# Kernel optimization log

Measured on AMD Instinct MI355X. Metric: run time of the kernel, lower is better.

Reference implementation:

```python
import jax, jax.numpy as jnp
import numpy as np

B, T, D, H = 4, 2048, 1024, 16
DH = D // H


def setup_inputs() -> dict:
    key = jax.random.key(0)
    ks = jax.random.split(key, 5)
    x = jax.random.normal(ks[0], (B, T, D), dtype=jnp.float32)
    W_qkv = jax.random.normal(ks[1], (D, 3 * D), dtype=jnp.float32) * 0.02
    b_qkv = jax.random.normal(ks[2], (3 * D,), dtype=jnp.float32) * 0.02
    W_o = jax.random.normal(ks[3], (D, D), dtype=jnp.float32) * 0.02
    b_o = jax.random.normal(ks[4], (D,), dtype=jnp.float32) * 0.02
    return {"x": x, "W_qkv": W_qkv, "b_qkv": b_qkv, "W_o": W_o, "b_o": b_o}


def reference(x, W_qkv, b_qkv, W_o, b_o):
    b, t, d = x.shape
    qkv = x @ W_qkv + b_qkv                      # [b, t, 3*d]
    # 'b t (k h dh) -> k b h t dh'
    qkv = qkv.reshape(b, t, 3, H, DH).transpose(2, 0, 3, 1, 4)
    q, k, v = qkv[0], qkv[1], qkv[2]             # each [b, h, t, dh]
    scores = jnp.einsum('bhqd,bhkd->bhqk', q, k) / jnp.sqrt(jnp.float32(DH))
    causal_mask = jnp.triu(jnp.ones((t, t), dtype=bool), k=1)  # True above diag
    scores = jnp.where(causal_mask, -jnp.inf, scores)
    attn = jax.nn.softmax(scores, axis=-1)       # [b, h, t, t]
    o = jnp.einsum('bhqk,bhkd->bqhd', attn, v).reshape(b, t, d)
    return o @ W_o + b_o
```

## Files before the change

kernel.cpp:

```cpp
#include <hip/hip_runtime.h>
#include <hip/hip_bf16.h>

typedef __attribute__((ext_vector_type(8))) short bh8;
typedef __attribute__((ext_vector_type(4))) float f32x4;

#define GBL(p) (const __attribute__((address_space(1))) void*)(p)
#define LDSP(p) (__attribute__((address_space(3))) void*)(p)

__device__ __forceinline__ ushort f2bf(float f){
  union { float f; unsigned u; } v; v.f = f;
  unsigned u = v.u;
  return (ushort)((u + 0x7fffu + ((u >> 16) & 1u)) >> 16);
}

__global__ __launch_bounds__(256) void cast_x_kernel(const float4* __restrict__ in,
                                                     ushort* __restrict__ out){
  int i = blockIdx.x * 256 + threadIdx.x;
  float4 v = in[i];
  ushort4 o;
  o.x = f2bf(v.x); o.y = f2bf(v.y); o.z = f2bf(v.z); o.w = f2bf(v.w);
  *(ushort4*)&out[(size_t)i * 4] = o;
}

__global__ __launch_bounds__(256) void transpose_cast_kernel(const float* __restrict__ in,
                                                             ushort* __restrict__ out,
                                                             int R, int C){
  __shared__ float tile[32][33];
  int bx = blockIdx.x * 32;
  int by = blockIdx.y * 32;
  int tx = threadIdx.x, ty = threadIdx.y;
  #pragma unroll
  for (int i = 0; i < 32; i += 8)
    tile[ty + i][tx] = in[(size_t)(by + ty + i) * C + bx + tx];
  __syncthreads();
  #pragma unroll
  for (int i = 0; i < 32; i += 8)
    out[(size_t)(bx + ty + i) * R + by + tx] = f2bf(tile[tx][ty + i]);
}

__global__ __launch_bounds__(256) void gemm_qkv_kernel(
    const ushort* __restrict__ A,
    const ushort* __restrict__ Bt,
    const float* __restrict__ bias,
    ushort* __restrict__ Qd, ushort* __restrict__ Kd, ushort* __restrict__ Vt)
{
  constexpr int K = 1024;
  __shared__ ushort sA[8192];
  __shared__ ushort sB[8192];
  const int tid = threadIdx.x;
  const int lane = tid & 63, wave = tid >> 6;
  const int quad = lane >> 4, l16 = lane & 15;
  const int rx7 = l16 & 7;
  const int wm = (wave >> 1) * 64, wn = (wave & 1) * 64;
  const size_t aBase = (size_t)blockIdx.x * 128 * K;
  const size_t bBase = (size_t)blockIdx.y * 128 * K;
  f32x4 acc[4][4] = {};
  for (int k0 = 0; k0 < K; k0 += 64){
    #pragma unroll
    for (int c = 0; c < 4; c++){
      int u = c * 256 + tid;
      int row = u >> 3, cu = (u & 7) ^ (row & 7);
      __builtin_amdgcn_global_load_lds(GBL(A + aBase + (size_t)row * K + k0 + cu * 8),
                                       LDSP(&sA[u * 8]), 16, 0, 0);
      __builtin_amdgcn_global_load_lds(GBL(Bt + bBase + (size_t)row * K + k0 + cu * 8),
                                       LDSP(&sB[u * 8]), 16, 0, 0);
    }
    __syncthreads();
    #pragma unroll
    for (int ks = 0; ks < 2; ks++){
      bh8 af[4], bf[4];
      #pragma unroll
      for (int i = 0; i < 4; i++){
        int row = wm + i * 16 + l16;
        af[i] = *(const bh8*)&sA[row * 64 + (((ks * 4 + quad) ^ rx7) << 3)];
      }
      #pragma unroll
      for (int j = 0; j < 4; j++){
        int row = wn + j * 16 + l16;
        bf[j] = *(const bh8*)&sB[row * 64 + (((ks * 4 + quad) ^ rx7) << 3)];
      }
      #pragma unroll
      for (int i = 0; i < 4; i++)
        #pragma unroll
        for (int j = 0; j < 4; j++)
          acc[i][j] = __builtin_amdgcn_mfma_f32_16x16x32_bf16(af[i], bf[j], acc[i][j], 0, 0, 0);
    }
    __syncthreads();
  }
  const int whichBlk = (blockIdx.y * 128) >> 10;
  #pragma unroll
  for (int i = 0; i < 4; i++){
    int mg = blockIdx.x * 128 + wm + i * 16 + quad * 4;
    int bb = mg >> 11, t0 = mg & 2047;
    #pragma unroll
    for (int j = 0; j < 4; j++){
      int ng = blockIdx.y * 128 + wn + j * 16 + l16;
      float bv = bias[ng];
      int h = (ng >> 6) & 15;
      int dh = ng & 63;
      if (whichBlk == 2){
        ushort4 o;
        o.x = f2bf(acc[i][j][0] + bv);
        o.y = f2bf(acc[i][j][1] + bv);
        o.z = f2bf(acc[i][j][2] + bv);
        o.w = f2bf(acc[i][j][3] + bv);
        *(ushort4*)&Vt[((size_t)((bb * 16 + h) * 64 + dh)) * 2048 + t0] = o;
      } else {
        ushort* dst = (whichBlk == 0) ? Qd : Kd;
        float sc = (whichBlk == 0) ? 0.18033688f : 1.0f;
        #pragma unroll
        for (int r = 0; r < 4; r++)
          dst[((size_t)((bb * 16 + h) * 2048 + t0 + r) << 6) + dh] = f2bf((acc[i][j][r] + bv) * sc);
      }
    }
  }
}

__global__ __launch_bounds__(256, 4) void flash_attn_kernel(
    const ushort* __restrict__ Qd, const ushort* __restrict__ Kd,
    const ushort* __restrict__ Vt, ushort* __restrict__ Od)
{
  __shared__ ushort sK[2][4096];
  __shared__ ushort sV[2][4096];
  __shared__ ushort sP[4][1024];
  const int tid = threadIdx.x;
  const int lane = tid & 63, wave = tid >> 6;
  const int quad = lane >> 4, l16 = lane & 15;
  const int bh = blockIdx.x, pairI = blockIdx.y;
  const size_t base = (size_t)bh * (2048 * 64);
  const float SINIT = -7.2134752f;

  const int p0 = tid, p1 = 256 + tid;
  const int r0 = p0 >> 3, c0 = (p0 & 7) ^ (r0 & 7);
  const int r1 = p1 >> 3, c1 = (p1 & 7) ^ (r1 & 7);
  const ushort* kp0 = Kd + base + r0 * 64 + c0 * 8;
  const ushort* kp1 = Kd + base + r1 * 64 + c1 * 8;
  const ushort* vp0 = Vt + base + (size_t)r0 * 2048 + c0 * 8;
  const ushort* vp1 = Vt + base + (size_t)r1 * 2048 + c1 * 8;

  const int b = bh >> 4, h = bh & 15;

  #pragma unroll 1
  for (int phase = 0; phase < 2; phase++){
    const int qt = phase ? pairI : (31 - pairI);
    const ushort* qrow = Qd + base + (size_t)(qt * 64 + wave * 16 + l16) * 64 + quad * 8;
    bh8 qf0 = *(const bh8*)qrow;
    bh8 qf1 = *(const bh8*)(qrow + 32);

    f32x4 Oacc[4] = {};
    float lpart[4] = {0.f, 0.f, 0.f, 0.f};

    __syncthreads();
    __builtin_amdgcn_global_load_lds(GBL(kp0), LDSP(&sK[0][p0 * 8]), 16, 0, 0);
    __builtin_amdgcn_global_load_lds(GBL(kp1), LDSP(&sK[0][p1 * 8]), 16, 0, 0);
    __builtin_amdgcn_global_load_lds(GBL(vp0), LDSP(&sV[0][p0 * 8]), 16, 0, 0);
    __builtin_amdgcn_global_load_lds(GBL(vp1), LDSP(&sV[0][p1 * 8]), 16, 0, 0);

    #pragma unroll 1
    for (int kt = 0; kt <= qt; kt++){
      const int buf = kt & 1;
      __syncthreads();
      if (kt < qt){
        const int nb = buf ^ 1;
        __builtin_amdgcn_global_load_lds(GBL(kp0 + (kt + 1) * 4096), LDSP(&sK[nb][p0 * 8]), 16, 0, 0);
        __builtin_amdgcn_global_load_lds(GBL(kp1 + (kt + 1) * 4096), LDSP(&sK[nb][p1 * 8]), 16, 0, 0);
        __builtin_amdgcn_global_load_lds(GBL(vp0 + (kt + 1) * 64),   LDSP(&sV[nb][p0 * 8]), 16, 0, 0);
        __builtin_amdgcn_global_load_lds(GBL(vp1 + (kt + 1) * 64),   LDSP(&sV[nb][p1 * 8]), 16, 0, 0);
      }
      f32x4 S[4];
      #pragma unroll
      for (int j = 0; j < 4; j++) S[j] = (f32x4){SINIT, SINIT, SINIT, SINIT};
      #pragma unroll
      for (int ks = 0; ks < 2; ks++){
        bh8 aq = ks ? qf1 : qf0;
        #pragma unroll
        for (int j = 0; j < 4; j++){
          int row = j * 16 + l16;
          int u = row * 8 + ((ks * 4 + quad) ^ (row & 7));
          bh8 bk = *(const bh8*)&sK[buf][u * 8];
          S[j] = __builtin_amdgcn_mfma_f32_16x16x32_bf16(aq, bk, S[j], 0, 0, 0);
        }
      }
      if (kt == qt){
        #pragma unroll
        for (int j = 0; j < 4; j++)
          #pragma unroll
          for (int r = 0; r < 4; r++){
            int relq = wave * 16 + quad * 4 + r;
            int relt = j * 16 + l16;
            if (relt > relq) S[j][r] = -1e30f;
          }
      }
      #pragma unroll
      for (int j = 0; j < 4; j++){
        float pv[4];
        #pragma unroll
        for (int r = 0; r < 4; r++){
          pv[r] = exp2f(S[j][r]);
          lpart[r] += pv[r];
        }
        __hip_bfloat162 pk0 = __float22bfloat162_rn({pv[0], pv[1]});
        __hip_bfloat162 pk1 = __float22bfloat162_rn({pv[2], pv[3]});
        ushort2 w0 = *(ushort2*)&pk0, w1 = *(ushort2*)&pk1;
        ushort w[4] = {w0.x, w0.y, w1.x, w1.y};
        #pragma unroll
        for (int r = 0; r < 4; r++){
          int row = quad * 4 + r;
          int cu = 2 * j + (l16 >> 3);
          int phys = row * 8 + (cu ^ (row & 7));
          sP[wave][phys * 8 + (l16 & 7)] = w[r];
        }
      }
      #pragma unroll
      for (int ks = 0; ks < 2; ks++){
        int up = l16 * 8 + ((ks * 4 + quad) ^ (l16 & 7));
        bh8 ap = *(const bh8*)&sP[wave][up * 8];
        #pragma unroll
        for (int j = 0; j < 4; j++){
          int row = j * 16 + l16;
          int u = row * 8 + ((ks * 4 + quad) ^ (row & 7));
          bh8 bv = *(const bh8*)&sV[buf][u * 8];
          Oacc[j] = __builtin_amdgcn_mfma_f32_16x16x32_bf16(ap, bv, Oacc[j], 0, 0, 0);
        }
      }
    }
    float lr[4];
    #pragma unroll
    for (int r = 0; r < 4; r++){
      float s = lpart[r];
      s += __shfl_xor(s, 1, 64);
      s += __shfl_xor(s, 2, 64);
      s += __shfl_xor(s, 4, 64);
      s += __shfl_xor(s, 8, 64);
      lr[r] = 1.0f / s;
    }
    #pragma unroll
    for (int j = 0; j < 4; j++)
      #pragma unroll
      for (int r = 0; r < 4; r++){
        int qg = qt * 64 + wave * 16 + quad * 4 + r;
        int dh = j * 16 + l16;
        Od[(size_t)(b * 2048 + qg) * 1024 + h * 64 + dh] = f2bf(Oacc[j][r] * lr[r]);
      }
  }
}

__global__ __launch_bounds__(256) void gemm_out_kernel(
    const ushort* __restrict__ A,
    const ushort* __restrict__ Bt,
    const float* __restrict__ bias,
    float* __restrict__ out)
{
  constexpr int K = 1024;
  __shared__ ushort sA[8192];
  __shared__ ushort sB[4096];
  const int tid = threadIdx.x;
  const int lane = tid & 63, wave = tid >> 6;
  const int quad = lane >> 4, l16 = lane & 15;
  const int rx7 = l16 & 7;
  const int wm = (wave >> 1) * 64, wn = (wave & 1) * 32;
  const size_t aBase = (size_t)blockIdx.x * 128 * K;
  const size_t bBase = (size_t)blockIdx.y * 64 * K;
  f32x4 acc[4][2] = {};
  for (int k0 = 0; k0 < K; k0 += 64){
    #pragma unroll
    for (int c = 0; c < 4; c++){
      int u = c * 256 + tid;
      int row = u >> 3, cu = (u & 7) ^ (row & 7);
      __builtin_amdgcn_global_load_lds(GBL(A + aBase + (size_t)row * K + k0 + cu * 8),
                                       LDSP(&sA[u * 8]), 16, 0, 0);
    }
    #pragma unroll
    for (int c = 0; c < 2; c++){
      int u = c * 256 + tid;
      int row = u >> 3, cu = (u & 7) ^ (row & 7);
      __builtin_amdgcn_global_load_lds(GBL(Bt + bBase + (size_t)row * K + k0 + cu * 8),
                                       LDSP(&sB[u * 8]), 16, 0, 0);
    }
    __syncthreads();
    #pragma unroll
    for (int ks = 0; ks < 2; ks++){
      bh8 af[4], bf[2];
      #pragma unroll
      for (int i = 0; i < 4; i++){
        int row = wm + i * 16 + l16;
        af[i] = *(const bh8*)&sA[row * 64 + (((ks * 4 + quad) ^ rx7) << 3)];
      }
      #pragma unroll
      for (int j = 0; j < 2; j++){
        int row = wn + j * 16 + l16;
        bf[j] = *(const bh8*)&sB[row * 64 + (((ks * 4 + quad) ^ rx7) << 3)];
      }
      #pragma unroll
      for (int i = 0; i < 4; i++)
        #pragma unroll
        for (int j = 0; j < 2; j++)
          acc[i][j] = __builtin_amdgcn_mfma_f32_16x16x32_bf16(af[i], bf[j], acc[i][j], 0, 0, 0);
    }
    __syncthreads();
  }
  #pragma unroll
  for (int i = 0; i < 4; i++){
    int gm = blockIdx.x * 128 + wm + i * 16 + quad * 4;
    #pragma unroll
    for (int j = 0; j < 2; j++){
      int ng = blockIdx.y * 64 + wn + j * 16 + l16;
      float bv = bias[ng];
      #pragma unroll
      for (int r = 0; r < 4; r++)
        out[(size_t)(gm + r) * 1024 + ng] = acc[i][j][r] + bv;
    }
  }
}

extern "C" void kernel_launch(void* const* d_in, const int* in_sizes, int n_in,
                              void* d_out, int out_size, void* d_ws, size_t ws_size,
                              hipStream_t stream) {
  const float* x    = (const float*)d_in[0];
  const float* Wqkv = (const float*)d_in[1];
  const float* bqkv = (const float*)d_in[2];
  const float* Wo   = (const float*)d_in[3];
  const float* bo   = (const float*)d_in[4];
  float* out = (float*)d_out;

  char* p = (char*)d_ws;
  ushort* xb  = (ushort*)p;
  ushort* WqT = (ushort*)(p + 16777216);
  ushort* WoT = (ushort*)(p + 16777216 + 6291456);
  ushort* Qd  = (ushort*)(p + 25165824);
  ushort* Kd  = (ushort*)(p + 25165824 + 16777216);
  ushort* Vt  = (ushort*)(p + 25165824 + 33554432);
  ushort* Od  = xb;

  cast_x_kernel<<<8192, 256, 0, stream>>>((const float4*)x, xb);
  transpose_cast_kernel<<<dim3(96, 32), dim3(32, 8), 0, stream>>>(Wqkv, WqT, 1024, 3072);
  transpose_cast_kernel<<<dim3(32, 32), dim3(32, 8), 0, stream>>>(Wo, WoT, 1024, 1024);
  gemm_qkv_kernel<<<dim3(64, 24), 256, 0, stream>>>(xb, WqT, bqkv, Qd, Kd, Vt);
  flash_attn_kernel<<<dim3(64, 16), 256, 0, stream>>>(Qd, Kd, Vt, Od);
  gemm_out_kernel<<<dim3(64, 16), 256, 0, stream>>>(Od, WoT, bo, out);
}
```

Before: 261.1 us.

## Compute transposed scores to keep P in registers, dropping LDS round-trip

The QK^T MFMA now swaps its operands so each lane holds scores for one query row across key positions. The bf16 probabilities can then feed a 16x16x16 MFMA directly as the B operand against V, with no write to and read back from the per-wave sP LDS buffer. The row-sum reduction shrinks to two cross-quad shuffles, and the output is written as packed 4-element stores. The trade is twice as many smaller MFMA instructions for the PV product and narrower 8-byte LDS reads of V, in exchange for less LDS traffic, less LDS footprint and no intra-wave LDS dependency.

New measurement: 288.1 us. 1.1x slower.

```diff
diff --git a/kernel.cpp b/kernel.cpp
--- a/kernel.cpp
+++ b/kernel.cpp
@@ -2,10 +2,17 @@
 #include <hip/hip_bf16.h>
 
 typedef __attribute__((ext_vector_type(8))) short bh8;
+typedef __attribute__((ext_vector_type(4))) short bh4;
 typedef __attribute__((ext_vector_type(4))) float f32x4;
 
 #define GBL(p) (const __attribute__((address_space(1))) void*)(p)
 #define LDSP(p) (__attribute__((address_space(3))) void*)(p)
+
+#if __has_builtin(__builtin_amdgcn_mfma_f32_16x16x16_bf16)
+#define MFMA16(a, b, c) __builtin_amdgcn_mfma_f32_16x16x16_bf16(a, b, c, 0, 0, 0)
+#else
+#define MFMA16(a, b, c) __builtin_amdgcn_mfma_f32_16x16x16bf16_1k(a, b, c, 0, 0, 0)
+#endif
 
 __device__ __forceinline__ ushort f2bf(float f){
   union { float f; unsigned u; } v; v.f = f;
@@ -122,7 +129,6 @@
 {
   __shared__ ushort sK[2][4096];
   __shared__ ushort sV[2][4096];
-  __shared__ ushort sP[4][1024];
   const int tid = threadIdx.x;
   const int lane = tid & 63, wave = tid >> 6;
   const int quad = lane >> 4, l16 = lane & 15;
@@ -148,7 +154,7 @@
     bh8 qf1 = *(const bh8*)(qrow + 32);
 
     f32x4 Oacc[4] = {};
-    float lpart[4] = {0.f, 0.f, 0.f, 0.f};
+    float lsum = 0.f;
 
     __syncthreads();
     __builtin_amdgcn_global_load_lds(GBL(kp0), LDSP(&sK[0][p0 * 8]), 16, 0, 0);
@@ -172,76 +178,61 @@
       for (int j = 0; j < 4; j++) S[j] = (f32x4){SINIT, SINIT, SINIT, SINIT};
       #pragma unroll
       for (int ks = 0; ks < 2; ks++){
-        bh8 aq = ks ? qf1 : qf0;
+        bh8 qk = ks ? qf1 : qf0;
         #pragma unroll
         for (int j = 0; j < 4; j++){
           int row = j * 16 + l16;
           int u = row * 8 + ((ks * 4 + quad) ^ (row & 7));
           bh8 bk = *(const bh8*)&sK[buf][u * 8];
-          S[j] = __builtin_amdgcn_mfma_f32_16x16x32_bf16(aq, bk, S[j], 0, 0, 0);
+          S[j] = __builtin_amdgcn_mfma_f32_16x16x32_bf16(bk, qk, S[j], 0, 0, 0);
         }
       }
       if (kt == qt){
+        const int relq = wave * 16 + l16;
         #pragma unroll
         for (int j = 0; j < 4; j++)
           #pragma unroll
           for (int r = 0; r < 4; r++){
-            int relq = wave * 16 + quad * 4 + r;
-            int relt = j * 16 + l16;
+            int relt = j * 16 + quad * 4 + r;
             if (relt > relq) S[j][r] = -1e30f;
           }
       }
+      bh4 pf[4];
       #pragma unroll
       for (int j = 0; j < 4; j++){
-        float pv[4];
-        #pragma unroll
-        for (int r = 0; r < 4; r++){
-          pv[r] = exp2f(S[j][r]);
-          lpart[r] += pv[r];
+        float pv0 = exp2f(S[j][0]), pv1 = exp2f(S[j][1]);
+        float pv2 = exp2f(S[j][2]), pv3 = exp2f(S[j][3]);
+        lsum += (pv0 + pv1) + (pv2 + pv3);
+        __hip_bfloat162 k0 = __float22bfloat162_rn({pv0, pv1});
+        __hip_bfloat162 k1 = __float22bfloat162_rn({pv2, pv3});
+        ushort2 w0 = *(ushort2*)&k0, w1 = *(ushort2*)&k1;
+        pf[j] = (bh4){(short)w0.x, (short)w0.y, (short)w1.x, (short)w1.y};
+      }
+      #pragma unroll
+      for (int mt = 0; mt < 4; mt++){
+        int row = mt * 16 + l16;
+        #pragma unroll
+        for (int j = 0; j < 4; j++){
+          int cu = j * 2 + (quad >> 1);
+          int idx = (row * 8 + (cu ^ (row & 7))) * 8 + (quad & 1) * 4;
+          bh4 vf = *(const bh4*)&sV[buf][idx];
+          Oacc[mt] = MFMA16(vf, pf[j], Oacc[mt]);
         }
-        __hip_bfloat162 pk0 = __float22bfloat162_rn({pv[0], pv[1]});
-        __hip_bfloat162 pk1 = __float22bfloat162_rn({pv[2], pv[3]});
-        ushort2 w0 = *(ushort2*)&pk0, w1 = *(ushort2*)&pk1;
-        ushort w[4] = {w0.x, w0.y, w1.x, w1.y};
-        #pragma unroll
-        for (int r = 0; r < 4; r++){
-          int row = quad * 4 + r;
-          int cu = 2 * j + (l16 >> 3);
-          int phys = row * 8 + (cu ^ (row & 7));
-          sP[wave][phys * 8 + (l16 & 7)] = w[r];
-        }
-      }
-      #pragma unroll
-      for (int ks = 0; ks < 2; ks++){
-        int up = l16 * 8 + ((ks * 4 + quad) ^ (l16 & 7));
-        bh8 ap = *(const bh8*)&sP[wave][up * 8];
-        #pragma unroll
-        for (int j = 0; j < 4; j++){
-          int row = j * 16 + l16;
-          int u = row * 8 + ((ks * 4 + quad) ^ (row & 7));
-          bh8 bv = *(const bh8*)&sV[buf][u * 8];
-          Oacc[j] = __builtin_amdgcn_mfma_f32_16x16x32_bf16(ap, bv, Oacc[j], 0, 0, 0);
-        }
-      }
-    }
-    float lr[4];
-    #pragma unroll
-    for (int r = 0; r < 4; r++){
-      float s = lpart[r];
-      s += __shfl_xor(s, 1, 64);
-      s += __shfl_xor(s, 2, 64);
-      s += __shfl_xor(s, 4, 64);
-      s += __shfl_xor(s, 8, 64);
-      lr[r] = 1.0f / s;
-    }
-    #pragma unroll
-    for (int j = 0; j < 4; j++)
-      #pragma unroll
-      for (int r = 0; r < 4; r++){
-        int qg = qt * 64 + wave * 16 + quad * 4 + r;
-        int dh = j * 16 + l16;
-        Od[(size_t)(b * 2048 + qg) * 1024 + h * 64 + dh] = f2bf(Oacc[j][r] * lr[r]);
-      }
+      }
+    }
+    lsum += __shfl_xor(lsum, 16, 64);
+    lsum += __shfl_xor(lsum, 32, 64);
+    float lr = 1.0f / lsum;
+    int qg = qt * 64 + wave * 16 + l16;
+    size_t obase = (size_t)(b * 2048 + qg) * 1024 + h * 64 + quad * 4;
+    #pragma unroll
+    for (int mt = 0; mt < 4; mt++){
+      __hip_bfloat162 k0 = __float22bfloat162_rn({Oacc[mt][0] * lr, Oacc[mt][1] * lr});
+      __hip_bfloat162 k1 = __float22bfloat162_rn({Oacc[mt][2] * lr, Oacc[mt][3] * lr});
+      ushort2 w0 = *(ushort2*)&k0, w1 = *(ushort2*)&k1;
+      ushort4 o = {w0.x, w0.y, w1.x, w1.y};
+      *(ushort4*)&Od[obase + mt * 16] = o;
+    }
   }
 }
 
```
